# Kernel optimization log

Hardware: AMD Instinct MI355X
Metric: run time of the kernel (lower is better)

The kernel has to match this reference:

```python
import jax, jax.numpy as jnp
import numpy as np

B, T, C = 256, 1024, 128
D = C // 2          # split_len1 == split_len2 == 64
CLAMP = 5.0


def setup_inputs() -> dict:
    key = jax.random.key(0)
    ks = jax.random.split(key, 13)
    p = lambda k, s: jax.random.normal(k, s, dtype=jnp.float32) * 0.1
    inp = {"x": jax.random.normal(ks[0], (B, T, C), dtype=jnp.float32)}
    for i, name in enumerate(["s1", "s2"]):
        b = 1 + i * 6
        inp[name + "_Wx"] = p(ks[b], (D, 3 * D))
        inp[name + "_Wh"] = p(ks[b + 1], (D, 3 * D))
        inp[name + "_bx"] = p(ks[b + 2], (3 * D,))
        inp[name + "_bh"] = p(ks[b + 3], (3 * D,))
        inp[name + "_Wo"] = p(ks[b + 4], (D, 2 * D))
        inp[name + "_bo"] = p(ks[b + 5], (2 * D,))
    return inp


def _gru(x, h, Wx, Wh, bx, bh, Wo, bo):
    # GRU cell with hidden size == input size, plus output projection (F_GRU).
    gx = x @ Wx + bx
    gh = h @ Wh + bh
    rx, zx, nx = jnp.split(gx, 3, axis=-1)
    rh, zh, nh = jnp.split(gh, 3, axis=-1)
    r = jax.nn.sigmoid(rx + rh)
    z = jax.nn.sigmoid(zx + zh)
    n = jnp.tanh(nx + r * nh)
    h_next = (1.0 - z) * n + z * h
    return h_next @ Wo + bo, h_next


def _e(s):
    # exp(clamp * 0.636 * atan(s / clamp)) -- soft-clamped scale
    return jnp.exp(CLAMP * 0.636 * jnp.arctan(s / CLAMP))


def reference(x, s1_Wx, s1_Wh, s1_bx, s1_bh, s1_Wo, s1_bo,
              s2_Wx, s2_Wh, s2_bx, s2_bh, s2_Wo, s2_bo):
    def step(carry, x_t):
        h1, h2 = carry
        x1, x2 = x_t[:, :D], x_t[:, D:]
        r2, h2n = _gru(x2, h2, s2_Wx, s2_Wh, s2_bx, s2_bh, s2_Wo, s2_bo)
        s2v, t2 = r2[:, :D], r2[:, D:]
        y1 = _e(s2v) * x1 + t2
        r1, h1n = _gru(y1, h1, s1_Wx, s1_Wh, s1_bx, s1_bh, s1_Wo, s1_bo)
        s1v, t1 = r1[:, :D], r1[:, D:]
        y2 = _e(s1v) * x2 + t1
        return (h1n, h2n), jnp.concatenate([y1, y2], axis=-1)

    h0 = (jnp.zeros((x.shape[0], D), x.dtype), jnp.zeros((x.shape[0], D), x.dtype))
    _, ys = jax.lax.scan(step, h0, jnp.swapaxes(x, 0, 1))  # scan over T
    return jnp.swapaxes(ys, 0, 1)  # [B, T, C]
```

## Files before the change

### kernel.cpp

```cpp
#include <hip/hip_runtime.h>

#define NB 256
#define NT 1024
#define NC 128
#define ND 64
#define SP 4
#define NSL 8
#define NJ 260

typedef _Float16 f16x8 __attribute__((ext_vector_type(8)));
typedef float f32x4 __attribute__((ext_vector_type(4)));

__device__ __forceinline__ float fexp2(float x){
#if __has_builtin(__builtin_amdgcn_exp2f)
  return __builtin_amdgcn_exp2f(x);
#else
  return exp2f(x);
#endif
}
__device__ __forceinline__ float frcp_(float x){
#if __has_builtin(__builtin_amdgcn_rcpf)
  return __builtin_amdgcn_rcpf(x);
#else
  return 1.0f / x;
#endif
}
__device__ __forceinline__ float sigmoid_f(float x){
  return frcp_(1.0f + fexp2(-1.4426950408889634f * x));
}
__device__ __forceinline__ float tanh_f(float x){
  return 1.0f - 2.0f * frcp_(fexp2(2.8853900817779268f * x) + 1.0f);
}
__device__ __forceinline__ float e_func(float s){
  float u = 0.2f * s;
  float au = fabsf(u);
  bool inv = au > 1.0f;
  float v = inv ? frcp_(au) : au;
  float v2 = v * v;
  float pp = -0.0117212f;
  pp = pp * v2 + 0.05265332f;
  pp = pp * v2 - 0.11643287f;
  pp = pp * v2 + 0.19354346f;
  pp = pp * v2 - 0.33262347f;
  pp = pp * v2 + 0.99997726f;
  float at = pp * v;
  if (inv) at = 1.5707963267948966f - at;
  at = __builtin_copysignf(at, u);
  return fexp2(4.5877702301963f * at);
}

#define BAR() asm volatile("s_waitcnt lgkmcnt(0)\n\ts_barrier" ::: "memory")

__device__ __forceinline__ f16x8 ldaf(const _Float16* pack, int lane, int ks){
  return *reinterpret_cast<const f16x8*>(
      reinterpret_cast<const char*>(pack) + 16*(lane>>4) + 64*ks);
}
__device__ __forceinline__ f16x8 bld(const float* __restrict__ W, int ldw,
                                     int ks, int tile, int lane){
  f16x8 v;
  const int kb = ks*32 + 8*(lane>>4);
  const int c  = tile*16 + (lane&15);
  #pragma unroll
  for (int j = 0; j < 8; ++j) v[j] = (_Float16)W[(kb + j)*ldw + c];
  return v;
}
__device__ __forceinline__ float sel4(float a0, float a1, float a2, float a3, int lane){
  float t01 = (lane & 16) ? a1 : a0;
  float t23 = (lane & 16) ? a3 : a2;
  return (lane & 32) ? t23 : t01;
}
#define MFMA16(acc, a, bfr) acc = __builtin_amdgcn_mfma_f32_16x16x32_f16(a, bfr, acc, 0, 0, 0)

__device__ __forceinline__ float dpp_xor1(float v){
  int r = __builtin_amdgcn_update_dpp(0, __builtin_bit_cast(int, v),
                                      0xB1 , 0xF, 0xF, true);
  return __builtin_bit_cast(float, r);
}

__device__ __forceinline__ void redist(float h, int lane, const int* addrs,
                                       f16x8* a0, f16x8* a1){
  float hsw = dpp_xor1(h);
  float lo = (lane & 1) ? hsw : h;
  float hp = (lane & 1) ? h : hsw;
  int pd = __builtin_bit_cast(int, __builtin_amdgcn_cvt_pkrtz(lo, hp));
  int d[8];
  #pragma unroll
  for (int q = 0; q < 8; ++q) d[q] = __builtin_amdgcn_ds_bpermute(addrs[q], pd);
  union { int u[4]; f16x8 v; } u0, u1;
  u0.u[0]=d[0]; u0.u[1]=d[1]; u0.u[2]=d[2]; u0.u[3]=d[3];
  u1.u[0]=d[4]; u1.u[1]=d[5]; u1.u[2]=d[6]; u1.u[3]=d[7];
  *a0 = u0.v; *a1 = u1.v;
}

__global__ __launch_bounds__(384, 1)
void glow_gru_kernel(const float* __restrict__ x,
                     const float* __restrict__ Wx1, const float* __restrict__ Wh1,
                     const float* __restrict__ bx1, const float* __restrict__ bh1,
                     const float* __restrict__ Wo1, const float* __restrict__ bo1,
                     const float* __restrict__ Wx2, const float* __restrict__ Wh2,
                     const float* __restrict__ bx2, const float* __restrict__ bh2,
                     const float* __restrict__ Wo2, const float* __restrict__ bo2,
                     float* __restrict__ out)
{
  __shared__ __align__(16) _Float16 x2p[NSL][64];
  __shared__ __align__(16) _Float16 h2p[NSL][64];
  __shared__ __align__(16) _Float16 y1p[NSL][64];
  __shared__ __align__(16) _Float16 h1p[NSL][64];
  __shared__ float px2[NSL][192];
  __shared__ float py1[NSL][192];

  const int l = threadIdx.x;
  const int w = l >> 6;
  const int i = l & 63;
  const int b = blockIdx.x;
  const long xbase = (long)b * NT * NC;

  if (l < 64){ h2p[NSL-1][l] = (_Float16)0.f; h1p[NSL-1][l] = (_Float16)0.f; }

  if (w == 0){
    f16x8 bf[12][2];
    #pragma unroll
    for (int t = 0; t < 12; ++t){ bf[t][0] = bld(Wx2,192,0,t,i); bf[t][1] = bld(Wx2,192,1,t,i); }
    float xg[SP], xn[SP];
    #pragma unroll
    for (int s = 0; s < SP; ++s){
      x2p[s][i] = (_Float16)x[xbase + (long)s*NC + 64 + i];
      xg[s] = x[xbase + (long)(SP+s)*NC + 64 + i];
    }
    __syncthreads();
    for (int J = 0; J <= NJ; ++J){
      const int t0 = SP*J;
      #pragma unroll
      for (int s = 0; s < SP; ++s){
        const int tt = SP*(J+2) + s;
        xn[s] = (tt < NT) ? x[xbase + (long)tt*NC + 64 + i] : 0.f;
      }
      if (t0 < NT){
        #pragma unroll
        for (int s = 0; s < SP; ++s){
          const int t = t0 + s;
          f16x8 a0 = ldaf(x2p[t&(NSL-1)], i, 0);
          f16x8 a1 = ldaf(x2p[t&(NSL-1)], i, 1);
          f32x4 acc[12];
          f32x4 zz = {0.f,0.f,0.f,0.f};
          #pragma unroll
          for (int t2 = 0; t2 < 12; ++t2){ acc[t2] = zz; MFMA16(acc[t2], a0, bf[t2][0]); }
          #pragma unroll
          for (int t2 = 0; t2 < 12; ++t2){ MFMA16(acc[t2], a1, bf[t2][1]); }
          if (i < 16){
            #pragma unroll
            for (int t2 = 0; t2 < 12; ++t2) px2[t&(NSL-1)][t2*16 + i] = acc[t2][0];
          }
        }
        const int tn0 = SP*(J+1);
        if (tn0 < NT){
          #pragma unroll
          for (int s = 0; s < SP; ++s) x2p[(tn0+s)&(NSL-1)][i] = (_Float16)xg[s];
        }
        #pragma unroll
        for (int s = 0; s < SP; ++s) xg[s] = xn[s];
      }
      BAR();
    }
  } else if (w == 1){
    f16x8 bf[12][2];
    #pragma unroll
    for (int t = 0; t < 12; ++t){ bf[t][0] = bld(Wx1,192,0,t,i); bf[t][1] = bld(Wx1,192,1,t,i); }
    __syncthreads();
    for (int J = 0; J <= NJ; ++J){
      const int t0 = SP*(J-3);
      if (t0 >= 0 && t0 < NT){
        #pragma unroll
        for (int s = 0; s < SP; ++s){
          const int t = t0 + s;
          f16x8 a0 = ldaf(y1p[t&(NSL-1)], i, 0);
          f16x8 a1 = ldaf(y1p[t&(NSL-1)], i, 1);
          f32x4 acc[12];
          f32x4 zz = {0.f,0.f,0.f,0.f};
          #pragma unroll
          for (int t2 = 0; t2 < 12; ++t2){ acc[t2] = zz; MFMA16(acc[t2], a0, bf[t2][0]); }
          #pragma unroll
          for (int t2 = 0; t2 < 12; ++t2){ MFMA16(acc[t2], a1, bf[t2][1]); }
          if (i < 16){
            #pragma unroll
            for (int t2 = 0; t2 < 12; ++t2) py1[t&(NSL-1)][t2*16 + i] = acc[t2][0];
          }
        }
      }
      BAR();
    }
  } else if (w == 2 || w == 3){
    const bool isA = (w == 2);
    const float* WH = isA ? Wh2 : Wh1;
    const float* bx = isA ? bx2 : bx1;
    const float* bh = isA ? bh2 : bh1;
    _Float16 (*hr)[64] = isA ? h2p : h1p;
    float (*pr)[192]   = isA ? px2 : py1;
    const int lag = isA ? 1 : 4;
    f16x8 bf[12][2];
    #pragma unroll
    for (int t = 0; t < 12; ++t){ bf[t][0] = bld(WH,192,0,t,i); bf[t][1] = bld(WH,192,1,t,i); }
    int addrs[8];
    #pragma unroll
    for (int q = 0; q < 8; ++q) addrs[q] = 8*(16*(q>>2) + 4*(i>>4) + (q&3));
    const float b0 = bx[i] + bh[i];
    const float b1 = bx[64+i] + bh[64+i];
    const float b2v = bx[128+i], b3v = bh[128+i];
    float h = 0.f;
    __syncthreads();
    for (int J = 0; J <= NJ; ++J){
      const int t0 = SP*(J - lag);
      if (t0 >= 0 && t0 < NT){
        float rxs[SP], zxs[SP], nxs[SP];
        #pragma unroll
        for (int s = 0; s < SP; ++s){
          rxs[s] = pr[(t0+s)&(NSL-1)][i];
          zxs[s] = pr[(t0+s)&(NSL-1)][64+i];
          nxs[s] = pr[(t0+s)&(NSL-1)][128+i];
        }
        #pragma unroll
        for (int s = 0; s < SP; ++s){
          const int t = t0 + s;
          f16x8 a0, a1;
          redist(h, i, addrs, &a0, &a1);
          f32x4 accA[12], accB[12];
          f32x4 zz = {0.f,0.f,0.f,0.f};
          #pragma unroll
          for (int t2 = 0; t2 < 12; ++t2){ accA[t2] = zz; MFMA16(accA[t2], a0, bf[t2][0]); }
          #pragma unroll
          for (int t2 = 0; t2 < 12; ++t2){ accB[t2] = zz; MFMA16(accB[t2], a1, bf[t2][1]); }
          float rh = sel4(accA[0][0]+accB[0][0], accA[1][0]+accB[1][0],
                          accA[2][0]+accB[2][0], accA[3][0]+accB[3][0], i);
          float r = sigmoid_f(rxs[s] + rh + b0);
          float zh = sel4(accA[4][0]+accB[4][0], accA[5][0]+accB[5][0],
                          accA[6][0]+accB[6][0], accA[7][0]+accB[7][0], i);
          float z = sigmoid_f(zxs[s] + zh + b1);
          float nh = sel4(accA[8][0]+accB[8][0], accA[9][0]+accB[9][0],
                          accA[10][0]+accB[10][0], accA[11][0]+accB[11][0], i);
          float nn = tanh_f(nxs[s] + b2v + r*(nh + b3v));
          h = (1.f - z)*nn + z*h;
          hr[t&(NSL-1)][i] = (_Float16)h;
        }
      }
      BAR();
    }
  } else {
    const bool isB = (w == 4);
    const float* WO = isB ? Wo2 : Wo1;
    const float* bo = isB ? bo2 : bo1;
    _Float16 (*hr)[64] = isB ? h2p : h1p;
    const int lag  = isB ? 2 : 5;
    const int xoff = isB ? 0 : 64;
    f16x8 bf[8][2];
    #pragma unroll
    for (int t = 0; t < 8; ++t){ bf[t][0] = bld(WO,128,0,t,i); bf[t][1] = bld(WO,128,1,t,i); }
    const float b0 = bo[i], b1 = bo[64+i];
    float xg[SP], xn[SP];
    #pragma unroll
    for (int s = 0; s < SP; ++s) xg[s] = x[xbase + (long)s*NC + xoff + i];
    __syncthreads();
    for (int J = 0; J <= NJ; ++J){
      const int t0 = SP*(J - lag);
      #pragma unroll
      for (int s = 0; s < SP; ++s){
        const int tt = t0 + SP + s;
        xn[s] = (tt >= 0 && tt < NT) ? x[xbase + (long)tt*NC + xoff + i] : 0.f;
      }
      if (t0 >= 0 && t0 < NT){
        #pragma unroll
        for (int s = 0; s < SP; ++s){
          const int t = t0 + s;
          f16x8 a0 = ldaf(hr[t&(NSL-1)], i, 0);
          f16x8 a1 = ldaf(hr[t&(NSL-1)], i, 1);
          f32x4 acc[8];
          f32x4 zz = {0.f,0.f,0.f,0.f};
          #pragma unroll
          for (int t2 = 0; t2 < 8; ++t2){ acc[t2] = zz; MFMA16(acc[t2], a0, bf[t2][0]); }
          #pragma unroll
          for (int t2 = 0; t2 < 8; ++t2){ MFMA16(acc[t2], a1, bf[t2][1]); }
          float sv = sel4(acc[0][0], acc[1][0], acc[2][0], acc[3][0], i);
          float tv = sel4(acc[4][0], acc[5][0], acc[6][0], acc[7][0], i);
          float y = e_func(sv + b0) * xg[s] + (tv + b1);
          out[xbase + (long)t*NC + xoff + i] = y;
          if (isB) y1p[t&(NSL-1)][i] = (_Float16)y;
        }
        #pragma unroll
        for (int s = 0; s < SP; ++s) xg[s] = xn[s];
      }
      BAR();
    }
  }
}

extern "C" void kernel_launch(void* const* d_in, const int* in_sizes, int n_in,
                              void* d_out, int out_size, void* d_ws, size_t ws_size,
                              hipStream_t stream) {
  const float* x   = (const float*)d_in[0];
  const float* Wx1 = (const float*)d_in[1];
  const float* Wh1 = (const float*)d_in[2];
  const float* bx1 = (const float*)d_in[3];
  const float* bh1 = (const float*)d_in[4];
  const float* Wo1 = (const float*)d_in[5];
  const float* bo1 = (const float*)d_in[6];
  const float* Wx2 = (const float*)d_in[7];
  const float* Wh2 = (const float*)d_in[8];
  const float* bx2 = (const float*)d_in[9];
  const float* bh2 = (const float*)d_in[10];
  const float* Wo2 = (const float*)d_in[11];
  const float* bo2 = (const float*)d_in[12];
  float* out = (float*)d_out;

  hipLaunchKernelGGL(glow_gru_kernel, dim3(NB), dim3(384), 0, stream,
                     x, Wx1, Wh1, bx1, bh1, Wo1, bo1,
                     Wx2, Wh2, bx2, bh2, Wo2, bo2, out);
}
```

Measured before the change: 437.4 us.

## Batch 16 timesteps per MFMA row block in the non-recurrent pipeline stages

The input-projection and output-projection waves now process 16 timesteps at once, using all 16 rows of each 16x16x32 MFMA. Previously they issued one mostly-empty MFMA per timestep and used only row 0. The x tile is loaded straight from global memory as float4 into the MFMA A operand, which removes the x2p staging ring. Ring buffers are enlarged to 32 slots with padded rows. This cuts MFMA count and barriers per timestep about fourfold. The recurrent GRU waves still step one timestep at a time but now sync only once every 16 steps. Risks include longer pipeline fill latency, LDS bank conflicts on the strided writes, and the removal of the h ring zero-initialisation.

```diff
diff --git a/kernel.cpp b/kernel.cpp
--- a/kernel.cpp
+++ b/kernel.cpp
@@ -4,9 +4,11 @@
 #define NT 1024
 #define NC 128
 #define ND 64
-#define SP 4
-#define NSL 8
-#define NJ 260
+#define SP 16
+#define NSL 32
+#define NJ 68
+#define PXW 196
+#define PHW 72
 
 typedef _Float16 f16x8 __attribute__((ext_vector_type(8)));
 typedef float f32x4 __attribute__((ext_vector_type(4)));
@@ -51,10 +53,6 @@
 
 #define BAR() asm volatile("s_waitcnt lgkmcnt(0)\n\ts_barrier" ::: "memory")
 
-__device__ __forceinline__ f16x8 ldaf(const _Float16* pack, int lane, int ks){
-  return *reinterpret_cast<const f16x8*>(
-      reinterpret_cast<const char*>(pack) + 16*(lane>>4) + 64*ks);
-}
 __device__ __forceinline__ f16x8 bld(const float* __restrict__ W, int ldw,
                                      int ks, int tile, int lane){
   f16x8 v;
@@ -64,6 +62,11 @@
   for (int j = 0; j < 8; ++j) v[j] = (_Float16)W[(kb + j)*ldw + c];
   return v;
 }
+__device__ __forceinline__ f16x8 ldafb(const _Float16* ring, int t0, int lane, int ks){
+  return *reinterpret_cast<const f16x8*>(
+      reinterpret_cast<const char*>(ring)
+      + (((t0 & (NSL-1)) + (lane & 15)) * (PHW*2)) + 16*(lane>>4) + 64*ks);
+}
 __device__ __forceinline__ float sel4(float a0, float a1, float a2, float a3, int lane){
   float t01 = (lane & 16) ? a1 : a0;
   float t23 = (lane & 16) ? a3 : a2;
@@ -73,10 +76,9 @@
 
 __device__ __forceinline__ float dpp_xor1(float v){
   int r = __builtin_amdgcn_update_dpp(0, __builtin_bit_cast(int, v),
-                                      0xB1 , 0xF, 0xF, true);
+                                      0xB1, 0xF, 0xF, true);
   return __builtin_bit_cast(float, r);
 }
-
 __device__ __forceinline__ void redist(float h, int lane, const int* addrs,
                                        f16x8* a0, f16x8* a1){
   float hsw = dpp_xor1(h);
@@ -91,6 +93,12 @@
   u1.u[0]=d[4]; u1.u[1]=d[5]; u1.u[2]=d[6]; u1.u[3]=d[7];
   *a0 = u0.v; *a1 = u1.v;
 }
+__device__ __forceinline__ f16x8 packx8(float4 u, float4 v){
+  f16x8 r;
+  r[0]=(_Float16)u.x; r[1]=(_Float16)u.y; r[2]=(_Float16)u.z; r[3]=(_Float16)u.w;
+  r[4]=(_Float16)v.x; r[5]=(_Float16)v.y; r[6]=(_Float16)v.z; r[7]=(_Float16)v.w;
+  return r;
+}
 
 __global__ __launch_bounds__(384, 1)
 void glow_gru_kernel(const float* __restrict__ x,
@@ -102,12 +110,11 @@
                      const float* __restrict__ Wo2, const float* __restrict__ bo2,
                      float* __restrict__ out)
 {
-  __shared__ __align__(16) _Float16 x2p[NSL][64];
-  __shared__ __align__(16) _Float16 h2p[NSL][64];
-  __shared__ __align__(16) _Float16 y1p[NSL][64];
-  __shared__ __align__(16) _Float16 h1p[NSL][64];
-  __shared__ float px2[NSL][192];
-  __shared__ float py1[NSL][192];
+  __shared__ __align__(16) _Float16 h2p[NSL][PHW];
+  __shared__ __align__(16) _Float16 y1p[NSL][PHW];
+  __shared__ __align__(16) _Float16 h1p[NSL][PHW];
+  __shared__ float px2[NSL][PXW];
+  __shared__ float py1[NSL][PXW];
 
   const int l = threadIdx.x;
   const int w = l >> 6;
@@ -115,50 +122,37 @@
   const int b = blockIdx.x;
   const long xbase = (long)b * NT * NC;
 
-  if (l < 64){ h2p[NSL-1][l] = (_Float16)0.f; h1p[NSL-1][l] = (_Float16)0.f; }
-
   if (w == 0){
     f16x8 bf[12][2];
     #pragma unroll
     for (int t = 0; t < 12; ++t){ bf[t][0] = bld(Wx2,192,0,t,i); bf[t][1] = bld(Wx2,192,1,t,i); }
-    float xg[SP], xn[SP];
-    #pragma unroll
-    for (int s = 0; s < SP; ++s){
-      x2p[s][i] = (_Float16)x[xbase + (long)s*NC + 64 + i];
-      xg[s] = x[xbase + (long)(SP+s)*NC + 64 + i];
-    }
+    const float* pxA = x + xbase + 64 + (long)(i & 15)*NC + 8*(i >> 4);
     __syncthreads();
     for (int J = 0; J <= NJ; ++J){
       const int t0 = SP*J;
-      #pragma unroll
-      for (int s = 0; s < SP; ++s){
-        const int tt = SP*(J+2) + s;
-        xn[s] = (tt < NT) ? x[xbase + (long)tt*NC + 64 + i] : 0.f;
-      }
       if (t0 < NT){
-        #pragma unroll
-        for (int s = 0; s < SP; ++s){
-          const int t = t0 + s;
-          f16x8 a0 = ldaf(x2p[t&(NSL-1)], i, 0);
-          f16x8 a1 = ldaf(x2p[t&(NSL-1)], i, 1);
-          f32x4 acc[12];
-          f32x4 zz = {0.f,0.f,0.f,0.f};
-          #pragma unroll
-          for (int t2 = 0; t2 < 12; ++t2){ acc[t2] = zz; MFMA16(acc[t2], a0, bf[t2][0]); }
-          #pragma unroll
-          for (int t2 = 0; t2 < 12; ++t2){ MFMA16(acc[t2], a1, bf[t2][1]); }
-          if (i < 16){
-            #pragma unroll
-            for (int t2 = 0; t2 < 12; ++t2) px2[t&(NSL-1)][t2*16 + i] = acc[t2][0];
-          }
-        }
-        const int tn0 = SP*(J+1);
-        if (tn0 < NT){
-          #pragma unroll
-          for (int s = 0; s < SP; ++s) x2p[(tn0+s)&(NSL-1)][i] = (_Float16)xg[s];
-        }
-        #pragma unroll
-        for (int s = 0; s < SP; ++s) xg[s] = xn[s];
+        const float* base = pxA + (long)t0*NC;
+        float4 u0 = *(const float4*)(base);
+        float4 u1 = *(const float4*)(base + 4);
+        float4 v0 = *(const float4*)(base + 32);
+        float4 v1 = *(const float4*)(base + 36);
+        f16x8 a0 = packx8(u0, u1);
+        f16x8 a1 = packx8(v0, v1);
+        f32x4 zz = {0.f,0.f,0.f,0.f};
+        f32x4 acc[12];
+        #pragma unroll
+        for (int t2 = 0; t2 < 12; ++t2){
+          acc[t2] = zz;
+          MFMA16(acc[t2], a0, bf[t2][0]);
+          MFMA16(acc[t2], a1, bf[t2][1]);
+        }
+        const int rb = (t0 + 4*(i>>4)) & (NSL-1);
+        #pragma unroll
+        for (int t2 = 0; t2 < 12; ++t2){
+          #pragma unroll
+          for (int rg = 0; rg < 4; ++rg)
+            px2[rb + rg][t2*16 + (i&15)] = acc[t2][rg];
+        }
       }
       BAR();
     }
@@ -170,21 +164,22 @@
     for (int J = 0; J <= NJ; ++J){
       const int t0 = SP*(J-3);
       if (t0 >= 0 && t0 < NT){
-        #pragma unroll
-        for (int s = 0; s < SP; ++s){
-          const int t = t0 + s;
-          f16x8 a0 = ldaf(y1p[t&(NSL-1)], i, 0);
-          f16x8 a1 = ldaf(y1p[t&(NSL-1)], i, 1);
-          f32x4 acc[12];
-          f32x4 zz = {0.f,0.f,0.f,0.f};
-          #pragma unroll
-          for (int t2 = 0; t2 < 12; ++t2){ acc[t2] = zz; MFMA16(acc[t2], a0, bf[t2][0]); }
-          #pragma unroll
-          for (int t2 = 0; t2 < 12; ++t2){ MFMA16(acc[t2], a1, bf[t2][1]); }
-          if (i < 16){
-            #pragma unroll
-            for (int t2 = 0; t2 < 12; ++t2) py1[t&(NSL-1)][t2*16 + i] = acc[t2][0];
-          }
+        f16x8 a0 = ldafb(&y1p[0][0], t0, i, 0);
+        f16x8 a1 = ldafb(&y1p[0][0], t0, i, 1);
+        f32x4 zz = {0.f,0.f,0.f,0.f};
+        f32x4 acc[12];
+        #pragma unroll
+        for (int t2 = 0; t2 < 12; ++t2){
+          acc[t2] = zz;
+          MFMA16(acc[t2], a0, bf[t2][0]);
+          MFMA16(acc[t2], a1, bf[t2][1]);
+        }
+        const int rb = (t0 + 4*(i>>4)) & (NSL-1);
+        #pragma unroll
+        for (int t2 = 0; t2 < 12; ++t2){
+          #pragma unroll
+          for (int rg = 0; rg < 4; ++rg)
+            py1[rb + rg][t2*16 + (i&15)] = acc[t2][rg];
         }
       }
       BAR();
@@ -194,8 +189,8 @@
     const float* WH = isA ? Wh2 : Wh1;
     const float* bx = isA ? bx2 : bx1;
     const float* bh = isA ? bh2 : bh1;
-    _Float16 (*hr)[64] = isA ? h2p : h1p;
-    float (*pr)[192]   = isA ? px2 : py1;
+    _Float16 (*hr)[PHW] = isA ? h2p : h1p;
+    float (*pr)[PXW]    = isA ? px2 : py1;
     const int lag = isA ? 1 : 4;
     f16x8 bf[12][2];
     #pragma unroll
@@ -248,44 +243,52 @@
     const bool isB = (w == 4);
     const float* WO = isB ? Wo2 : Wo1;
     const float* bo = isB ? bo2 : bo1;
-    _Float16 (*hr)[64] = isB ? h2p : h1p;
+    _Float16 (*hr)[PHW] = isB ? h2p : h1p;
     const int lag  = isB ? 2 : 5;
     const int xoff = isB ? 0 : 64;
     f16x8 bf[8][2];
     #pragma unroll
     for (int t = 0; t < 8; ++t){ bf[t][0] = bld(WO,128,0,t,i); bf[t][1] = bld(WO,128,1,t,i); }
-    const float b0 = bo[i], b1 = bo[64+i];
-    float xg[SP], xn[SP];
-    #pragma unroll
-    for (int s = 0; s < SP; ++s) xg[s] = x[xbase + (long)s*NC + xoff + i];
+    const int c = i & 15;
+    float bS[4], bT[4];
+    #pragma unroll
+    for (int t2 = 0; t2 < 4; ++t2){
+      bS[t2] = bo[t2*16 + c];
+      bT[t2] = bo[64 + t2*16 + c];
+    }
     __syncthreads();
     for (int J = 0; J <= NJ; ++J){
       const int t0 = SP*(J - lag);
-      #pragma unroll
-      for (int s = 0; s < SP; ++s){
-        const int tt = t0 + SP + s;
-        xn[s] = (tt >= 0 && tt < NT) ? x[xbase + (long)tt*NC + xoff + i] : 0.f;
-      }
       if (t0 >= 0 && t0 < NT){
-        #pragma unroll
-        for (int s = 0; s < SP; ++s){
-          const int t = t0 + s;
-          f16x8 a0 = ldaf(hr[t&(NSL-1)], i, 0);
-          f16x8 a1 = ldaf(hr[t&(NSL-1)], i, 1);
-          f32x4 acc[8];
-          f32x4 zz = {0.f,0.f,0.f,0.f};
-          #pragma unroll
-          for (int t2 = 0; t2 < 8; ++t2){ acc[t2] = zz; MFMA16(acc[t2], a0, bf[t2][0]); }
-          #pragma unroll
-          for (int t2 = 0; t2 < 8; ++t2){ MFMA16(acc[t2], a1, bf[t2][1]); }
-          float sv = sel4(acc[0][0], acc[1][0], acc[2][0], acc[3][0], i);
-          float tv = sel4(acc[4][0], acc[5][0], acc[6][0], acc[7][0], i);
-          float y = e_func(sv + b0) * xg[s] + (tv + b1);
-          out[xbase + (long)t*NC + xoff + i] = y;
-          if (isB) y1p[t&(NSL-1)][i] = (_Float16)y;
-        }
-        #pragma unroll
-        for (int s = 0; s < SP; ++s) xg[s] = xn[s];
+        float xv[4][4];
+        #pragma unroll
+        for (int t2 = 0; t2 < 4; ++t2){
+          #pragma unroll
+          for (int rg = 0; rg < 4; ++rg){
+            const int t = t0 + 4*(i>>4) + rg;
+            xv[t2][rg] = x[xbase + (long)t*NC + xoff + t2*16 + c];
+          }
+        }
+        f16x8 a0 = ldafb(&hr[0][0], t0, i, 0);
+        f16x8 a1 = ldafb(&hr[0][0], t0, i, 1);
+        f32x4 zz = {0.f,0.f,0.f,0.f};
+        f32x4 acc[8];
+        #pragma unroll
+        for (int t2 = 0; t2 < 8; ++t2){
+          acc[t2] = zz;
+          MFMA16(acc[t2], a0, bf[t2][0]);
+          MFMA16(acc[t2], a1, bf[t2][1]);
+        }
+        #pragma unroll
+        for (int t2 = 0; t2 < 4; ++t2){
+          #pragma unroll
+          for (int rg = 0; rg < 4; ++rg){
+            const int t = t0 + 4*(i>>4) + rg;
+            float y = e_func(acc[t2][rg] + bS[t2]) * xv[t2][rg] + (acc[t2+4][rg] + bT[t2]);
+            out[xbase + (long)t*NC + xoff + t2*16 + c] = y;
+            if (isB) y1p[t & (NSL-1)][t2*16 + c] = (_Float16)y;
+          }
+        }
       }
       BAR();
     }
```

After: 412.9 us. -5.6%, faster.
